# Performance work log

Measured on AMD Instinct MI355X. Metric: run time of the kernel, lower is better.

## Reference

```python
import jax, jax.numpy as jnp
import numpy as np

DIM, HEADS, LAYERS, HID = 1024, 16, 6, 4096
PAST_CTX, MAX_PERIOD = 1000, 10000.0
HEAD_DIM = DIM // HEADS


def _ln(x, g, b, eps=1e-5):
    m = jnp.mean(x, axis=-1, keepdims=True)
    v = jnp.mean((x - m) ** 2, axis=-1, keepdims=True)
    return (x - m) * jax.lax.rsqrt(v + eps) * g + b


def setup_inputs() -> dict:
    key = jax.random.key(0)
    ks = jax.random.split(key, 8)
    s = 0.02
    inp = {
        "x": jax.random.normal(ks[0], (2, 2048, DIM), jnp.float32),
        "norm_in_g": jnp.ones((DIM,), jnp.float32),
        "norm_in_b": jnp.zeros((DIM,), jnp.float32),
        "Wqkv": jax.random.normal(ks[1], (LAYERS, 3 * DIM, DIM), jnp.float32) * s,
        "bqkv": jnp.zeros((LAYERS, 3 * DIM), jnp.float32),
        "Wo": jax.random.normal(ks[2], (LAYERS, DIM, DIM), jnp.float32) * s,
        "bo": jnp.zeros((LAYERS, DIM), jnp.float32),
        "ln1_g": jnp.ones((LAYERS, DIM), jnp.float32),
        "ln1_b": jnp.zeros((LAYERS, DIM), jnp.float32),
        "ln2_g": jnp.ones((LAYERS, DIM), jnp.float32),
        "ln2_b": jnp.zeros((LAYERS, DIM), jnp.float32),
        "W1": jax.random.normal(ks[3], (LAYERS, HID, DIM), jnp.float32) * s,
        "b1": jnp.zeros((LAYERS, HID), jnp.float32),
        "W2": jax.random.normal(ks[4], (LAYERS, DIM, HID), jnp.float32) * s,
        "b2": jnp.zeros((LAYERS, DIM), jnp.float32),
    }
    return inp


def _forward(x, norm_in_g, norm_in_b, Wqkv, bqkv, Wo, bo, ln1_g, ln1_b, ln2_g, ln2_b, W1, b1, W2, b2):
    B, T, C = x.shape
    H = 1  # states=None -> per-layer zero cache of length 1
    # sinusoidal positional embedding (offset=0)
    half = C // 2
    positions = jnp.arange(T, dtype=jnp.float32)[None, :, None]  # [1,T,1]
    adim = jnp.arange(half, dtype=jnp.float32)[None, None, :]
    phase = positions / (MAX_PERIOD ** (adim / (half - 1)))
    pos_emb = jnp.concatenate([jnp.cos(phase), jnp.sin(phase)], axis=-1)  # [1,T,C]
    x = _ln(x, norm_in_g, norm_in_b) + pos_emb

    # sliding-window causal mask over keys [past(H) | current(T)]
    q_pos = jnp.arange(H, T + H)[:, None]
    k_pos = jnp.arange(T + H)[None, :]
    delta = q_pos - k_pos
    valid = (delta >= 0) & (delta <= PAST_CTX)  # [T, T+H]
    neg = jnp.finfo(x.dtype).min

    past = jnp.zeros((B, H, C), x.dtype)
    for l in range(LAYERS):
        # post-norm layer (norm_first=False)
        keys = jnp.concatenate([past, x], axis=1)  # [B,T+H,C]
        Wq, Wk, Wv = Wqkv[l][:C], Wqkv[l][C:2 * C], Wqkv[l][2 * C:]
        bq, bk, bv = bqkv[l][:C], bqkv[l][C:2 * C], bqkv[l][2 * C:]
        q = (x @ Wq.T + bq).reshape(B, T, HEADS, HEAD_DIM)
        k = (keys @ Wk.T + bk).reshape(B, T + H, HEADS, HEAD_DIM)
        v = (keys @ Wv.T + bv).reshape(B, T + H, HEADS, HEAD_DIM)
        scores = jnp.einsum('bqhd,bkhd->bhqk', q, k) / jnp.sqrt(jnp.asarray(HEAD_DIM, x.dtype))
        scores = jnp.where(valid[None, None], scores, neg)
        attn = jax.nn.softmax(scores, axis=-1)
        o = jnp.einsum('bhqk,bkhd->bqhd', attn, v).reshape(B, T, C)
        o = o @ Wo[l].T + bo[l]
        x = _ln(x + o, ln1_g[l], ln1_b[l])
        ff = jax.nn.gelu(x @ W1[l].T + b1[l], approximate=False) @ W2[l].T + b2[l]
        x = _ln(x + ff, ln2_g[l], ln2_b[l])
    return x


def reference(x, norm_in_g, norm_in_b, Wqkv, bqkv, Wo, bo, ln1_g, ln1_b, ln2_g, ln2_b, W1, b1, W2, b2):
    return _forward(x, norm_in_g, norm_in_b, Wqkv, bqkv, Wo, bo, ln1_g, ln1_b, ln2_g, ln2_b, W1, b1, W2, b2)
```

## Files before the change

kernel.cpp:

```cpp
#include <hip/hip_runtime.h>
#include <math.h>

typedef short short8 __attribute__((ext_vector_type(8)));
typedef float floatx4 __attribute__((ext_vector_type(4)));

__device__ __forceinline__ unsigned short f2bf(float f) {
  unsigned int u = __builtin_bit_cast(unsigned int, f);
  u = (u + 0x7FFFu + ((u >> 16) & 1u)) >> 16;
  return (unsigned short)u;
}

__device__ __forceinline__ unsigned int pack_bf2(float lo, float hi) {
  return (unsigned int)f2bf(lo) | ((unsigned int)f2bf(hi) << 16);
}

__device__ __forceinline__ void async16(const void* g, void* l) {
  __builtin_amdgcn_global_load_lds(
      (const __attribute__((address_space(1))) unsigned int*)g,
      (__attribute__((address_space(3))) unsigned int*)l, 16, 0, 0);
}

template <int EPI, int BM>
__global__ __launch_bounds__(512, 2) void gemm3(
    const unsigned short* __restrict__ A, const unsigned short* __restrict__ B,
    const float* __restrict__ bias, void* __restrict__ outp,
    int M, int N, int K) {
  constexpr int BN = 128;
  constexpr int ROWS = BM + BN;
  constexpr int BUFE = ROWS * 64;
  constexpr int NLT = ROWS / 64;
  constexpr int WM = BM / 64;
  constexpr int WN = 8 / WM;
  constexpr int NJ = (BN / WN) / 16;
  __shared__ unsigned short S[3 * BUFE];

  const int tid = threadIdx.x;
  const int lane = tid & 63, wid = tid >> 6;
  const int quad = lane >> 4, l15 = lane & 15;
  const int wm = wid / WN, wn = wid % WN;
  const int wmo = wm * 64;
  const int wno = wn * (BN / WN);

  const int gx = gridDim.x;
  const int nwg = gx * gridDim.y;
  int lin = blockIdx.y * gx + blockIdx.x;
  lin = (lin & 7) * (nwg >> 3) + (lin >> 3);
  const size_t m0 = (size_t)(lin / gx) * BM;
  const size_t n0 = (size_t)(lin % gx) * BN;

  auto stage = [&](int buf, int kt) {
#pragma unroll
    for (int l = 0; l < NLT; ++l) {
      int ci = l * 512 + tid;
      int r = ci >> 3;
      int c = (ci & 7) ^ (r & 7);
      const unsigned short* src =
          (r < BM) ? A + (m0 + r) * (size_t)K + kt + c * 8
                   : B + (n0 + (r - BM)) * (size_t)K + kt + c * 8;
      async16(src, &S[buf * BUFE + ci * 8]);
    }
  };

  floatx4 acc[4][NJ] = {};

  stage(0, 0);
  stage(1, 64);
  int cur = 0;

  for (int kt = 0; kt < K; kt += 64) {
    if (kt + 128 < K) {
      int nb = cur + 2;
      if (nb >= 3) nb -= 3;
      stage(nb, kt + 128);
      asm volatile("s_waitcnt vmcnt(%0)" ::"n"(2 * NLT) : "memory");
    } else if (kt + 64 < K) {
      asm volatile("s_waitcnt vmcnt(%0)" ::"n"(NLT) : "memory");
    } else {
      asm volatile("s_waitcnt vmcnt(0)" ::: "memory");
    }
    __builtin_amdgcn_s_barrier();
    __builtin_amdgcn_sched_barrier(0);

    short8 a[4][2], b[NJ][2];
    const unsigned short* Sc = &S[cur * BUFE];
#pragma unroll
    for (int i = 0; i < 4; ++i) {
      const int R = wmo + i * 16 + l15;
#pragma unroll
      for (int kh = 0; kh < 2; ++kh)
        a[i][kh] = *(const short8*)&Sc[R * 64 + (((kh * 4 + quad) ^ (R & 7)) * 8)];
    }
#pragma unroll
    for (int j = 0; j < NJ; ++j) {
      const int R = BM + wno + j * 16 + l15;
#pragma unroll
      for (int kh = 0; kh < 2; ++kh)
        b[j][kh] = *(const short8*)&Sc[R * 64 + (((kh * 4 + quad) ^ (R & 7)) * 8)];
    }
    asm volatile("s_waitcnt lgkmcnt(0)" ::: "memory");
    __builtin_amdgcn_sched_barrier(0);
    __builtin_amdgcn_s_barrier();

    __builtin_amdgcn_s_setprio(1);
#pragma unroll
    for (int kh = 0; kh < 2; ++kh)
#pragma unroll
      for (int i = 0; i < 4; ++i)
#pragma unroll
        for (int j = 0; j < NJ; ++j)
          acc[i][j] = __builtin_amdgcn_mfma_f32_16x16x32_bf16(
              a[i][kh], b[j][kh], acc[i][j], 0, 0, 0);
    __builtin_amdgcn_s_setprio(0);

    ++cur;
    if (cur >= 3) cur -= 3;
  }

#pragma unroll
  for (int j = 0; j < NJ; ++j) {
    const int n = (int)n0 + wno + j * 16 + l15;
    const float bv = bias[n];
    const float sc = (EPI == 3 && n < 1024) ? 0.125f : 1.0f;
#pragma unroll
    for (int i = 0; i < 4; ++i) {
      const int mbase = (int)m0 + wmo + i * 16 + quad * 4;
#pragma unroll
      for (int r = 0; r < 4; ++r) {
        float v = acc[i][j][r] + bv;
        if (EPI == 2) v = 0.5f * v * (1.0f + erff(v * 0.70710678f));
        if (EPI == 3) v *= sc;
        size_t idx = (size_t)(mbase + r) * (size_t)N + n;
        if (EPI == 1) ((float*)outp)[idx] = v;
        else ((unsigned short*)outp)[idx] = f2bf(v);
      }
    }
  }
}

__global__ __launch_bounds__(512) void attn_kernel(
    const unsigned short* __restrict__ qkv, const float* __restrict__ bqkv_l,
    unsigned short* __restrict__ attno) {
  __shared__ unsigned short Qs[128 * 64];
  __shared__ unsigned short Ks[64 * 64];
  __shared__ unsigned short Vt[64 * 72];
  __shared__ unsigned short Ps[8][16 * 72];
  __shared__ float Lsh[8][16];

  const int qt = blockIdx.x, h = blockIdx.y, b = blockIdx.z;
  const int qs = qt * 128;
  const int tid = threadIdx.x, lane = tid & 63, wid = tid >> 6;
  const int quad = lane >> 4, l15 = lane & 15;
  const size_t rowbase = (size_t)b * 2048;
  const int hoff = h * 64;

#pragma unroll
  for (int r = 0; r < 2; ++r) {
    int c = r * 512 + tid;
    int qrow = c >> 3, ccq = c & 7;
    async16(qkv + (rowbase + qs + qrow) * 3072 + hoff + ccq * 8, &Qs[c * 8]);
  }

  floatx4 oacc[4] = {};
  float lpart = 0.f;

  int kstart = qs - 999;
  if (kstart < 0) kstart = 0;
  kstart &= ~63;
  const int kend = qs + 128;

  const int krow = tid >> 3, cc = tid & 7;
  const int qlo = qs + wid * 16 + 1;
  const int qhi = qlo + 15;
  const int qpos = qs + wid * 16 + l15 + 1;

  for (int k0 = kstart; k0 <= kend; k0 += 64) {
    __syncthreads();
    {
      int xr = k0 + krow - 1;
      xr = xr < 0 ? 0 : (xr > 2047 ? 2047 : xr);
      async16(qkv + (rowbase + xr) * 3072 + 1024 + hoff + cc * 8, &Ks[tid * 8]);
    }
    {
      int xr = k0 + krow - 1;
      xr = xr < 0 ? 0 : (xr > 2047 ? 2047 : xr);
      short8 vv = *(const short8*)(qkv + (rowbase + xr) * 3072 + 2048 + hoff + cc * 8);
#pragma unroll
      for (int e = 0; e < 8; ++e) {
        int e2 = (e + cc) & 7;
        Vt[(cc * 8 + e2) * 72 + krow] = (unsigned short)vv[e2];
      }
    }
    if (k0 == 0) {
      __syncthreads();
      if (tid < 64) {
        Ks[tid] = f2bf(bqkv_l[1024 + hoff + tid]);
        Vt[tid * 72] = f2bf(bqkv_l[2048 + hoff + tid]);
      }
    }
    __syncthreads();

    if (k0 <= qhi && qlo - (k0 + 63) <= 1000) {
      floatx4 sacc[4] = {};
#pragma unroll
      for (int ks = 0; ks < 2; ++ks) {
        short8 bq = *(const short8*)&Qs[(wid * 16 + l15) * 64 + ks * 32 + quad * 8];
#pragma unroll
        for (int nj = 0; nj < 4; ++nj) {
          short8 ak = *(const short8*)&Ks[(nj * 16 + l15) * 64 + ks * 32 + quad * 8];
          sacc[nj] = __builtin_amdgcn_mfma_f32_16x16x32_bf16(ak, bq, sacc[nj], 0, 0, 0);
        }
      }

      const bool full = (k0 + 63 <= qlo) && (qhi - k0 <= 1000);
#pragma unroll
      for (int nj = 0; nj < 4; ++nj) {
        float e[4];
        if (full) {
#pragma unroll
          for (int r = 0; r < 4; ++r) e[r] = __expf(sacc[nj][r]);
        } else {
          const int keyb = k0 + nj * 16 + quad * 4;
#pragma unroll
          for (int r = 0; r < 4; ++r) {
            int delta = qpos - (keyb + r);
            e[r] = (delta >= 0 && delta <= 1000) ? __expf(sacc[nj][r]) : 0.f;
          }
        }
        lpart += (e[0] + e[1]) + (e[2] + e[3]);
        uint2 pk = make_uint2(pack_bf2(e[0], e[1]), pack_bf2(e[2], e[3]));
        *(uint2*)&Ps[wid][l15 * 72 + nj * 16 + quad * 4] = pk;
      }

#pragma unroll
      for (int ks = 0; ks < 2; ++ks) {
        short8 pf = *(const short8*)&Ps[wid][l15 * 72 + ks * 32 + quad * 8];
#pragma unroll
        for (int di = 0; di < 4; ++di) {
          short8 vf = *(const short8*)&Vt[(di * 16 + l15) * 72 + ks * 32 + quad * 8];
          oacc[di] = __builtin_amdgcn_mfma_f32_16x16x32_bf16(pf, vf, oacc[di], 0, 0, 0);
        }
      }
    }
  }

  lpart += __shfl_xor(lpart, 16);
  lpart += __shfl_xor(lpart, 32);
  if (quad == 0) Lsh[wid][l15] = lpart;
  __builtin_amdgcn_s_waitcnt(0);
  float linv[4];
#pragma unroll
  for (int r = 0; r < 4; ++r) linv[r] = 1.0f / Lsh[wid][quad * 4 + r];

#pragma unroll
  for (int di = 0; di < 4; ++di)
#pragma unroll
    for (int r = 0; r < 4; ++r) {
      int q = qs + wid * 16 + quad * 4 + r;
      attno[(rowbase + q) * 1024 + hoff + di * 16 + l15] =
          f2bf(oacc[di][r] * linv[r]);
    }
}

__global__ __launch_bounds__(256) void ln_first_kernel(
    const float* __restrict__ xin, const float* __restrict__ g,
    const float* __restrict__ bb, float* __restrict__ xout,
    unsigned short* __restrict__ xbout) {
  const int row = blockIdx.x, tid = threadIdx.x;
  const size_t base = (size_t)row * 1024 + tid * 4;
  float4 xv = *(const float4*)&xin[base];
  float s = xv.x + xv.y + xv.z + xv.w;
  float sq = xv.x * xv.x + xv.y * xv.y + xv.z * xv.z + xv.w * xv.w;
  __shared__ float red[8];
  for (int off = 32; off > 0; off >>= 1) { s += __shfl_down(s, off); sq += __shfl_down(sq, off); }
  if ((tid & 63) == 0) { red[tid >> 6] = s; red[4 + (tid >> 6)] = sq; }
  __syncthreads();
  s = red[0] + red[1] + red[2] + red[3];
  sq = red[4] + red[5] + red[6] + red[7];
  const float mean = s * (1.f / 1024.f);
  const float rstd = rsqrtf(sq * (1.f / 1024.f) - mean * mean + 1e-5f);
  float4 gv = *(const float4*)&g[tid * 4];
  float4 bv = *(const float4*)&bb[tid * 4];
  const float tf = (float)(row & 2047);
  float xs[4] = {xv.x, xv.y, xv.z, xv.w};
  float gs[4] = {gv.x, gv.y, gv.z, gv.w};
  float bs[4] = {bv.x, bv.y, bv.z, bv.w};
  float y[4];
#pragma unroll
  for (int e = 0; e < 4; ++e) {
    int c = tid * 4 + e;
    float a = (c < 512) ? (float)c : (float)(c - 512);
    float ph = tf * powf(10000.f, -a * (1.f / 511.f));
    float pe = (c < 512) ? cosf(ph) : sinf(ph);
    y[e] = (xs[e] - mean) * rstd * gs[e] + bs[e] + pe;
  }
  *(float4*)&xout[base] = make_float4(y[0], y[1], y[2], y[3]);
  *(ushort4*)&xbout[base] = make_ushort4(f2bf(y[0]), f2bf(y[1]), f2bf(y[2]), f2bf(y[3]));
}

__global__ __launch_bounds__(256) void ln_res_kernel(
    const float* __restrict__ xin, const float* __restrict__ addv,
    const float* __restrict__ g, const float* __restrict__ bb,
    float* __restrict__ xout, unsigned short* __restrict__ xbout) {
  const int row = blockIdx.x, tid = threadIdx.x;
  const size_t base = (size_t)row * 1024 + tid * 4;
  float4 xv = *(const float4*)&xin[base];
  float4 av = *(const float4*)&addv[base];
  float v0 = xv.x + av.x, v1 = xv.y + av.y, v2 = xv.z + av.z, v3 = xv.w + av.w;
  float s = v0 + v1 + v2 + v3;
  float sq = v0 * v0 + v1 * v1 + v2 * v2 + v3 * v3;
  __shared__ float red[8];
  for (int off = 32; off > 0; off >>= 1) { s += __shfl_down(s, off); sq += __shfl_down(sq, off); }
  if ((tid & 63) == 0) { red[tid >> 6] = s; red[4 + (tid >> 6)] = sq; }
  __syncthreads();
  s = red[0] + red[1] + red[2] + red[3];
  sq = red[4] + red[5] + red[6] + red[7];
  const float mean = s * (1.f / 1024.f);
  const float rstd = rsqrtf(sq * (1.f / 1024.f) - mean * mean + 1e-5f);
  float4 gv = *(const float4*)&g[tid * 4];
  float4 bv = *(const float4*)&bb[tid * 4];
  float vs[4] = {v0, v1, v2, v3};
  float gs[4] = {gv.x, gv.y, gv.z, gv.w};
  float bs[4] = {bv.x, bv.y, bv.z, bv.w};
  float y[4];
#pragma unroll
  for (int e = 0; e < 4; ++e) y[e] = (vs[e] - mean) * rstd * gs[e] + bs[e];
  *(float4*)&xout[base] = make_float4(y[0], y[1], y[2], y[3]);
  if (xbout)
    *(ushort4*)&xbout[base] = make_ushort4(f2bf(y[0]), f2bf(y[1]), f2bf(y[2]), f2bf(y[3]));
}

__global__ __launch_bounds__(256) void convw_kernel(
    const float* __restrict__ wqkv, const float* __restrict__ wo,
    const float* __restrict__ w1, const float* __restrict__ w2,
    unsigned short* __restrict__ dst) {
  for (int base = blockIdx.x * 256 + threadIdx.x; base < 3145728; base += 786432) {
    int i = base << 2;
    const float* src;
    int off;
    if (i < 3145728)      { src = wqkv; off = i; }
    else if (i < 4194304) { src = wo;   off = i - 3145728; }
    else if (i < 8388608) { src = w1;   off = i - 4194304; }
    else                  { src = w2;   off = i - 8388608; }
    float4 v = *(const float4*)&src[off];
    *(ushort4*)&dst[i] = make_ushort4(f2bf(v.x), f2bf(v.y), f2bf(v.z), f2bf(v.w));
  }
}

extern "C" void kernel_launch(void* const* d_in, const int* in_sizes, int n_in,
                              void* d_out, int out_size, void* d_ws, size_t ws_size,
                              hipStream_t stream) {
  const float* x    = (const float*)d_in[0];
  const float* ng   = (const float*)d_in[1];
  const float* nb   = (const float*)d_in[2];
  const float* Wqkv = (const float*)d_in[3];
  const float* bqkv = (const float*)d_in[4];
  const float* Wo   = (const float*)d_in[5];
  const float* bo   = (const float*)d_in[6];
  const float* ln1g = (const float*)d_in[7];
  const float* ln1b = (const float*)d_in[8];
  const float* ln2g = (const float*)d_in[9];
  const float* ln2b = (const float*)d_in[10];
  const float* W1   = (const float*)d_in[11];
  const float* b1   = (const float*)d_in[12];
  const float* W2   = (const float*)d_in[13];
  const float* b2   = (const float*)d_in[14];

  char* ws = (char*)d_ws;
  float* xf           = (float*)(ws + 0);
  unsigned short* xb  = (unsigned short*)(ws + 16777216);
  unsigned short* qkv = (unsigned short*)(ws + 25165824);
  unsigned short* att = (unsigned short*)(ws + 50331648);
  unsigned short* h1  = (unsigned short*)(ws + 58720256);
  float* gout         = (float*)(ws + 92274688);
  unsigned short* wb  = (unsigned short*)(ws + 109051904);
  unsigned short* wqkvb = wb;
  unsigned short* wob   = wb + 3145728;
  unsigned short* w1b   = wb + 4194304;
  unsigned short* w2b   = wb + 8388608;

  ln_first_kernel<<<4096, 256, 0, stream>>>(x, ng, nb, xf, xb);

  for (int l = 0; l < 6; ++l) {
    convw_kernel<<<3072, 256, 0, stream>>>(Wqkv + (size_t)l * 3145728,
                                           Wo + (size_t)l * 1048576,
                                           W1 + (size_t)l * 4194304,
                                           W2 + (size_t)l * 4194304, wb);
    gemm3<3, 256><<<dim3(24, 16), 512, 0, stream>>>(xb, wqkvb, bqkv + l * 3072, qkv,
                                                    4096, 3072, 1024);
    attn_kernel<<<dim3(16, 16, 2), 512, 0, stream>>>(qkv, bqkv + l * 3072, att);
    gemm3<1, 128><<<dim3(8, 32), 512, 0, stream>>>(att, wob, bo + l * 1024, gout,
                                                   4096, 1024, 1024);
    ln_res_kernel<<<4096, 256, 0, stream>>>(xf, gout, ln1g + l * 1024, ln1b + l * 1024,
                                            xf, xb);
    gemm3<2, 256><<<dim3(32, 16), 512, 0, stream>>>(xb, w1b, b1 + l * 4096, h1,
                                                    4096, 4096, 1024);
    gemm3<1, 128><<<dim3(8, 32), 512, 0, stream>>>(h1, w2b, b2 + l * 1024, gout,
                                                   4096, 1024, 4096);
    ln_res_kernel<<<4096, 256, 0, stream>>>(xf, gout, ln2g + l * 1024, ln2b + l * 1024,
                                            (l == 5) ? (float*)d_out : xf,
                                            (l == 5) ? nullptr : xb);
  }
}
```

Baseline: 1.752 ms.

## Double-buffer K/V tiles in attention with async LDS loads and XOR swizzle

```diff
diff --git a/kernel.cpp b/kernel.cpp
--- a/kernel.cpp
+++ b/kernel.cpp
@@ -141,7 +141,8 @@
     const unsigned short* __restrict__ qkv, const float* __restrict__ bqkv_l,
     unsigned short* __restrict__ attno) {
   __shared__ unsigned short Qs[128 * 64];
-  __shared__ unsigned short Ks[64 * 64];
+  __shared__ unsigned short Ks[2][64 * 64];
+  __shared__ unsigned short Vrow[2][64 * 64];
   __shared__ unsigned short Vt[64 * 72];
   __shared__ unsigned short Ps[8][16 * 72];
   __shared__ float Lsh[8][16];
@@ -157,7 +158,8 @@
   for (int r = 0; r < 2; ++r) {
     int c = r * 512 + tid;
     int qrow = c >> 3, ccq = c & 7;
-    async16(qkv + (rowbase + qs + qrow) * 3072 + hoff + ccq * 8, &Qs[c * 8]);
+    async16(qkv + (rowbase + qs + qrow) * 3072 + hoff + ((ccq ^ (qrow & 7)) * 8),
+            &Qs[c * 8]);
   }
 
   floatx4 oacc[4] = {};
@@ -173,40 +175,54 @@
   const int qhi = qlo + 15;
   const int qpos = qs + wid * 16 + l15 + 1;
 
+  auto stageKV = [&](int buf, int k0) {
+    int xr = k0 + krow - 1;
+    xr = xr < 0 ? 0 : (xr > 2047 ? 2047 : xr);
+    async16(qkv + (rowbase + xr) * 3072 + 1024 + hoff + ((cc ^ (krow & 7)) * 8),
+            &Ks[buf][tid * 8]);
+    async16(qkv + (rowbase + xr) * 3072 + 2048 + hoff + cc * 8,
+            &Vrow[buf][tid * 8]);
+  };
+
+  stageKV(0, kstart);
+  int cur = 0;
+
   for (int k0 = kstart; k0 <= kend; k0 += 64) {
-    __syncthreads();
+    if (k0 + 64 <= kend) {
+      stageKV(cur ^ 1, k0 + 64);
+      asm volatile("s_waitcnt vmcnt(2)" ::: "memory");
+    } else {
+      asm volatile("s_waitcnt vmcnt(0)" ::: "memory");
+    }
+    __builtin_amdgcn_s_barrier();
+    __builtin_amdgcn_sched_barrier(0);
+
+    if (k0 == 0) {
+      if (tid < 64) Ks[cur][tid] = f2bf(bqkv_l[1024 + hoff + tid]);
+      __syncthreads();
+    }
+
     {
-      int xr = k0 + krow - 1;
-      xr = xr < 0 ? 0 : (xr > 2047 ? 2047 : xr);
-      async16(qkv + (rowbase + xr) * 3072 + 1024 + hoff + cc * 8, &Ks[tid * 8]);
-    }
-    {
-      int xr = k0 + krow - 1;
-      xr = xr < 0 ? 0 : (xr > 2047 ? 2047 : xr);
-      short8 vv = *(const short8*)(qkv + (rowbase + xr) * 3072 + 2048 + hoff + cc * 8);
+      short8 vv = *(const short8*)&Vrow[cur][tid * 8];
 #pragma unroll
       for (int e = 0; e < 8; ++e) {
         int e2 = (e + cc) & 7;
         Vt[(cc * 8 + e2) * 72 + krow] = (unsigned short)vv[e2];
       }
-    }
-    if (k0 == 0) {
-      __syncthreads();
-      if (tid < 64) {
-        Ks[tid] = f2bf(bqkv_l[1024 + hoff + tid]);
-        Vt[tid * 72] = f2bf(bqkv_l[2048 + hoff + tid]);
-      }
-    }
-    __syncthreads();
-
-    if (k0 <= qhi && qlo - (k0 + 63) <= 1000) {
+      if (k0 == 0 && tid < 64) Vt[tid * 72] = f2bf(bqkv_l[2048 + hoff + tid]);
+    }
+
+    const bool act = (k0 <= qhi) && (qlo - (k0 + 63) <= 1000);
+    if (act) {
       floatx4 sacc[4] = {};
 #pragma unroll
       for (int ks = 0; ks < 2; ++ks) {
-        short8 bq = *(const short8*)&Qs[(wid * 16 + l15) * 64 + ks * 32 + quad * 8];
+        short8 bq = *(const short8*)&Qs[(wid * 16 + l15) * 64 +
+                                        (((ks * 4 + quad) ^ (l15 & 7)) * 8)];
 #pragma unroll
         for (int nj = 0; nj < 4; ++nj) {
-          short8 ak = *(const short8*)&Ks[(nj * 16 + l15) * 64 + ks * 32 + quad * 8];
+          short8 ak = *(const short8*)&Ks[cur][(nj * 16 + l15) * 64 +
+                                              (((ks * 4 + quad) ^ (l15 & 7)) * 8)];
           sacc[nj] = __builtin_amdgcn_mfma_f32_16x16x32_bf16(ak, bq, sacc[nj], 0, 0, 0);
         }
       }
@@ -230,7 +246,14 @@
         uint2 pk = make_uint2(pack_bf2(e[0], e[1]), pack_bf2(e[2], e[3]));
         *(uint2*)&Ps[wid][l15 * 72 + nj * 16 + quad * 4] = pk;
       }
-
+    }
+
+    asm volatile("s_waitcnt lgkmcnt(0)" ::: "memory");
+    __builtin_amdgcn_sched_barrier(0);
+    __builtin_amdgcn_s_barrier();
+    __builtin_amdgcn_sched_barrier(0);
+
+    if (act) {
 #pragma unroll
       for (int ks = 0; ks < 2; ++ks) {
         short8 pf = *(const short8*)&Ps[wid][l15 * 72 + ks * 32 + quad * 8];
@@ -241,6 +264,7 @@
         }
       }
     }
+    cur ^= 1;
   }
 
   lpart += __shfl_xor(lpart, 16);
@@ -394,8 +418,8 @@
                                             xf, xb);
     gemm3<2, 256><<<dim3(32, 16), 512, 0, stream>>>(xb, w1b, b1 + l * 4096, h1,
                                                     4096, 4096, 1024);
-    gemm3<1, 128><<<dim3(8, 32), 512, 0, stream>>>(h1, w2b, b2 + l * 1024, gout,
-                                                   4096, 1024, 4096);
+    gemm3<1, 64 + 64><<<dim3(8, 32), 512, 0, stream>>>(h1, w2b, b2 + l * 1024, gout,
+                                                       4096, 1024, 4096);
     ln_res_kernel<<<4096, 256, 0, stream>>>(xf, gout, ln2g + l * 1024, ln2b + l * 1024,
                                             (l == 5) ? (float*)d_out : xf,
                                             (l == 5) ? nullptr : xb);
```

Result: no change. 1.739 ms (-0.8%).
